# Performance work log

Measured on AMD Instinct MI355X. Metric: run time of the kernel, lower is better.

## Reference

```python
import jax, jax.numpy as jnp
import numpy as np

N_NODES = 100000
N_EDGES = 1600000


def _sage_layer(x, src, dst, Wl, bl, Wr):
    # PyG SAGEConv (aggr='mean', root_weight=True):
    #   out_i = lin_l(mean_{j in N(i)} x_j) + lin_r(x_i)
    msg = x[src]                                              # [E, d] gather
    summed = jax.ops.segment_sum(msg, dst, num_segments=N_NODES)
    cnt = jax.ops.segment_sum(jnp.ones((src.shape[0],), x.dtype), dst,
                              num_segments=N_NODES)
    mean = summed / jnp.maximum(cnt, 1.0)[:, None]            # zero-deg nodes -> 0
    return mean @ Wl + bl + x @ Wr


def setup_inputs() -> dict:
    key = jax.random.key(0)
    ks = jax.random.split(key, 12)
    d_in, d_h, d_out = 6, 128, 64

    def lin(k, fi, fo):
        s = 1.0 / np.sqrt(fi)
        return jax.random.uniform(k, (fi, fo), jnp.float32, -s, s)

    return {
        "x": jax.random.normal(ks[0], (N_NODES, 10), jnp.float32),
        "edge_index": jax.random.randint(ks[1], (2, N_EDGES), 0, N_NODES),
        "Wl0": lin(ks[2], d_in, d_h), "bl0": jnp.zeros((d_h,), jnp.float32),
        "Wr0": lin(ks[3], d_in, d_h),
        "Wl1": lin(ks[4], d_h, d_h), "bl1": jnp.zeros((d_h,), jnp.float32),
        "Wr1": lin(ks[5], d_h, d_h),
        "Wl2": lin(ks[6], d_h, d_out), "bl2": jnp.zeros((d_out,), jnp.float32),
        "Wr2": lin(ks[7], d_h, d_out),
    }


def reference(x, edge_index, Wl0, bl0, Wr0, Wl1, bl1, Wr1, Wl2, bl2, Wr2):
    src, dst = edge_index[0], edge_index[1]
    h = x[:, 4:10]                                            # bus feature slice
    h = jax.nn.relu(_sage_layer(h, src, dst, Wl0, bl0, Wr0))
    h = jax.nn.relu(_sage_layer(h, src, dst, Wl1, bl1, Wr1))
    h = jax.nn.relu(_sage_layer(h, src, dst, Wl2, bl2, Wr2))
    return h
```

## Files before the change

kernel.cpp:

```cpp
#include <hip/hip_runtime.h>


typedef __attribute__((ext_vector_type(8))) short bf16x8;
typedef __attribute__((ext_vector_type(4))) float f32x4;
typedef __attribute__((ext_vector_type(2))) float f32x2;

constexpr int PB = 256;
constexpr int WTCH = 6144;
constexpr float F8SCALE = 32.0f;

static __device__ __forceinline__ int imax(int a, int b) { return a > b ? a : b; }

static __device__ __forceinline__ float bfbits_lo(unsigned u) {
    union { unsigned i; float f; } v; v.i = u << 16; return v.f;
}
static __device__ __forceinline__ float bfbits_hi(unsigned u) {
    union { unsigned i; float f; } v; v.i = u & 0xffff0000u; return v.f;
}
static __device__ __forceinline__ unsigned short f2bf(float f) {
    unsigned u = __float_as_uint(f);
    u = (u + 0x7fffu + ((u >> 16) & 1u)) >> 16;
    return (unsigned short)u;
}
static __device__ __forceinline__ unsigned pack2bf(float a, float b) {
    return (unsigned)f2bf(a) | ((unsigned)f2bf(b) << 16);
}
static __device__ __forceinline__ void acc_f8x4(unsigned u, float* a) {
    f32x2 lo = __builtin_amdgcn_cvt_pk_f32_fp8((int)u, false);
    f32x2 hi = __builtin_amdgcn_cvt_pk_f32_fp8((int)u, true);
    a[0] += lo[0]; a[1] += lo[1]; a[2] += hi[0]; a[3] += hi[1];
}
static __device__ __forceinline__ void acc_bf8(uint4 v, float* a) {
    a[0] += bfbits_lo(v.x); a[1] += bfbits_hi(v.x);
    a[2] += bfbits_lo(v.y); a[3] += bfbits_hi(v.y);
    a[4] += bfbits_lo(v.z); a[5] += bfbits_hi(v.z);
    a[6] += bfbits_lo(v.w); a[7] += bfbits_hi(v.w);
}


static __device__ __forceinline__ void wtfrag_katk(const float* __restrict__ W1,
                                                   const float* __restrict__ W2,
                                                   unsigned short* __restrict__ Wt,
                                                   int K1, int K, int N, int c) {
    int NB = N >> 4;
    int lane = c & 63;
    int n = (c >> 6) % NB;
    int ks = c / (NB << 6);
    int row = n * 16 + (lane & 15);
    int col = ks * 32 + (lane >> 4) * 8;
    unsigned short o[8];
#pragma unroll
    for (int j = 0; j < 8; ++j) {
        int k = col + j;
        float v = (k < K1) ? W1[k * N + row] : W2[(k - K1) * N + row];
        o[j] = f2bf(v);
    }
    *(uint4*)(Wt + (size_t)c * 8) = *(const uint4*)o;
}

static __device__ __forceinline__ void wtfrag_natn(const float* __restrict__ Wa,
                                                   const float* __restrict__ Wb,
                                                   unsigned short* __restrict__ Wt,
                                                   int K, int Nh, int c) {
    int NB = (2 * Nh) >> 4;
    int lane = c & 63;
    int n = (c >> 6) % NB;
    int ks = c / (NB << 6);
    int row = n * 16 + (lane & 15);
    int col = ks * 32 + (lane >> 4) * 8;
    unsigned short o[8];
#pragma unroll
    for (int j = 0; j < 8; ++j) {
        int k = col + j;
        float v = (row < Nh) ? Wa[k * Nh + row] : Wb[k * Nh + (row - Nh)];
        o[j] = f2bf(v);
    }
    *(uint4*)(Wt + (size_t)c * 8) = *(const uint4*)o;
}


__global__ __launch_bounds__(256) void k_prep(const float* __restrict__ Wl1,
                                              const float* __restrict__ Wr1,
                                              const float* __restrict__ Wl2,
                                              const float* __restrict__ Wr2,
                                              unsigned short* __restrict__ Wt1,
                                              unsigned short* __restrict__ Wt2,
                                              const int* __restrict__ dst,
                                              int* __restrict__ C,
                                              int nE, int nbk, int epb) {
    if (blockIdx.x < 24) {
        int c = blockIdx.x * 256 + threadIdx.x;
        if (c < 4096)        wtfrag_katk(Wl1, Wr1, Wt1, 128, 256, 128, c);
        else if (c < WTCH)   wtfrag_natn(Wl2, Wr2, Wt2, 128, 64, c - 4096);
        return;
    }
    __shared__ int h[512];
    int b = blockIdx.x - 24;
    for (int i = threadIdx.x; i < nbk; i += 256) h[i] = 0;
    __syncthreads();
    int e0 = b * epb;
    int e1 = min(e0 + epb, nE);
    for (int i = e0 + threadIdx.x; i < e1; i += 256)
        atomicAdd(&h[dst[i] >> 8], 1);
    __syncthreads();
    for (int i = threadIdx.x; i < nbk; i += 256)
        C[b * nbk + i] = h[i];
}


__global__ __launch_bounds__(256) void k_colscan(int* __restrict__ C,
                                                 int* __restrict__ tot, int nbk) {
    __shared__ int sm[256];
    int k = blockIdx.x, t = threadIdx.x;
    int v = C[t * nbk + k];
    sm[t] = v;
    __syncthreads();
    for (int o = 1; o < 256; o <<= 1) {
        int u = (t >= o) ? sm[t - o] : 0;
        __syncthreads();
        sm[t] += u;
        __syncthreads();
    }
    C[t * nbk + k] = sm[t] - v;
    if (t == 255) tot[k] = sm[255];
}

__global__ __launch_bounds__(256) void k_scan_a(const int* __restrict__ cnt,
                                                int* __restrict__ offs, int n) {
    __shared__ int sm[256];
    int t = threadIdx.x;
    int base = t * 4;
    int v0 = 0, v1 = 0, v2 = 0, v3 = 0;
    if (base + 3 < n) {
        int4 q = *(const int4*)(cnt + base);
        v0 = q.x; v1 = q.y; v2 = q.z; v3 = q.w;
    } else {
        if (base < n)     v0 = cnt[base];
        if (base + 1 < n) v1 = cnt[base + 1];
        if (base + 2 < n) v2 = cnt[base + 2];
    }
    int s = v0 + v1 + v2 + v3;
    sm[t] = s;
    __syncthreads();
    for (int o = 1; o < 256; o <<= 1) {
        int u = (t >= o) ? sm[t - o] : 0;
        __syncthreads();
        sm[t] += u;
        __syncthreads();
    }
    int excl = sm[t] - s;
    if (base < n)     offs[base]     = excl;
    if (base + 1 < n) offs[base + 1] = excl + v0;
    if (base + 2 < n) offs[base + 2] = excl + v0 + v1;
    if (base + 3 < n) offs[base + 3] = excl + v0 + v1 + v2;
    if (t == 255) offs[n] = sm[255];
}

__global__ __launch_bounds__(256) void k_p1fill(const int* __restrict__ src,
                                                const int* __restrict__ dst,
                                                const int* __restrict__ bstart,
                                                const int* __restrict__ C,
                                                unsigned* __restrict__ ebuf,
                                                int nE, int nbk, int epb) {
    __shared__ int cur[512];
    int b = blockIdx.x;
    for (int i = threadIdx.x; i < nbk; i += 256)
        cur[i] = bstart[i] + C[b * nbk + i];
    __syncthreads();
    int e0 = b * epb;
    int e1 = min(e0 + epb, nE);
    for (int i = e0 + threadIdx.x; i < e1; i += 256) {
        int d = dst[i];
        unsigned s = (unsigned)src[i];
        int p = atomicAdd(&cur[d >> 8], 1);
        ebuf[p] = (s << 8) | (unsigned)(d & 255);
    }
}

__global__ __launch_bounds__(256) void k_p2fill(const unsigned* __restrict__ ebuf,
                                                const int* __restrict__ bstart,
                                                int* __restrict__ offs,
                                                int* __restrict__ csr,
                                                int nN, int nE) {
    __shared__ int h[256], sm[256], cur[256];
    int k = blockIdx.x, t = threadIdx.x;
    int base = bstart[k], end = bstart[k + 1];
    h[t] = 0;
    __syncthreads();
    for (int i = base + t; i < end; i += 256)
        atomicAdd(&h[ebuf[i] & 255u], 1);
    __syncthreads();
    int v = h[t];
    sm[t] = v;
    __syncthreads();
    for (int o = 1; o < 256; o <<= 1) {
        int u = (t >= o) ? sm[t - o] : 0;
        __syncthreads();
        sm[t] += u;
        __syncthreads();
    }
    int excl = sm[t] - v;
    int node = (k << 8) + t;
    if (node < nN) offs[node] = base + excl;
    cur[t] = base + excl;
    if (k == 0 && t == 0) offs[nN] = nE;
    __syncthreads();
    for (int i = base + t; i < end; i += 256) {
        unsigned e = ebuf[i];
        int p = atomicAdd(&cur[e & 255u], 1);
        csr[p] = (int)(e >> 8);
    }
}


__global__ __launch_bounds__(256) void k_l0f(const float* __restrict__ x,
                                             const int* __restrict__ offs,
                                             const int* __restrict__ csr,
                                             const float* __restrict__ Wl,
                                             const float* __restrict__ bl,
                                             const float* __restrict__ Wr,
                                             unsigned short* __restrict__ out,
                                             unsigned char* __restrict__ out8, int nN) {
    int idx = blockIdx.x * 256 + threadIdx.x;
    int node = idx >> 4;
    int j = threadIdx.x & 15;
    if (node >= nN) return;
    int lo = offs[node], hi = offs[node + 1];
    float a0 = 0, a1 = 0, a2 = 0, a3 = 0, a4 = 0, a5 = 0;
    for (int e = lo + j; e < hi; e += 16) {
        int s = csr[e];
        const float* r = x + (size_t)s * 10 + 4;
        float2 v0 = *(const float2*)(r);
        float2 v1 = *(const float2*)(r + 2);
        float2 v2 = *(const float2*)(r + 4);
        a0 += v0.x; a1 += v0.y; a2 += v1.x; a3 += v1.y; a4 += v2.x; a5 += v2.y;
    }
#pragma unroll
    for (int mask = 1; mask < 16; mask <<= 1) {
        a0 += __shfl_xor(a0, mask); a1 += __shfl_xor(a1, mask);
        a2 += __shfl_xor(a2, mask); a3 += __shfl_xor(a3, mask);
        a4 += __shfl_xor(a4, mask); a5 += __shfl_xor(a5, mask);
    }
    float inv = 1.0f / (float)imax(hi - lo, 1);
    float m[6] = {a0 * inv, a1 * inv, a2 * inv, a3 * inv, a4 * inv, a5 * inv};
    const float* hp = x + (size_t)node * 10 + 4;
    float2 h01 = *(const float2*)hp, h23 = *(const float2*)(hp + 2), h45 = *(const float2*)(hp + 4);
    float h[6] = {h01.x, h01.y, h23.x, h23.y, h45.x, h45.y};
    int j0 = j * 8;
    float4 b0 = *(const float4*)(bl + j0);
    float4 b1 = *(const float4*)(bl + j0 + 4);
    float v[8] = {b0.x, b0.y, b0.z, b0.w, b1.x, b1.y, b1.z, b1.w};
#pragma unroll
    for (int k = 0; k < 6; ++k) {
        float4 w0 = *(const float4*)(Wl + k * 128 + j0);
        float4 w1 = *(const float4*)(Wl + k * 128 + j0 + 4);
        v[0] = fmaf(m[k], w0.x, v[0]); v[1] = fmaf(m[k], w0.y, v[1]);
        v[2] = fmaf(m[k], w0.z, v[2]); v[3] = fmaf(m[k], w0.w, v[3]);
        v[4] = fmaf(m[k], w1.x, v[4]); v[5] = fmaf(m[k], w1.y, v[5]);
        v[6] = fmaf(m[k], w1.z, v[6]); v[7] = fmaf(m[k], w1.w, v[7]);
    }
#pragma unroll
    for (int k = 0; k < 6; ++k) {
        float4 w0 = *(const float4*)(Wr + k * 128 + j0);
        float4 w1 = *(const float4*)(Wr + k * 128 + j0 + 4);
        v[0] = fmaf(h[k], w0.x, v[0]); v[1] = fmaf(h[k], w0.y, v[1]);
        v[2] = fmaf(h[k], w0.z, v[2]); v[3] = fmaf(h[k], w0.w, v[3]);
        v[4] = fmaf(h[k], w1.x, v[4]); v[5] = fmaf(h[k], w1.y, v[5]);
        v[6] = fmaf(h[k], w1.z, v[6]); v[7] = fmaf(h[k], w1.w, v[7]);
    }
#pragma unroll
    for (int t = 0; t < 8; ++t) v[t] = fmaxf(v[t], 0.f);
    unsigned ob[4];
#pragma unroll
    for (int t = 0; t < 4; ++t) ob[t] = pack2bf(v[2 * t], v[2 * t + 1]);
    *(uint4*)(out + (size_t)node * 128 + j0) = *(const uint4*)ob;
    int d0 = __builtin_amdgcn_cvt_pk_fp8_f32(v[0] * F8SCALE, v[1] * F8SCALE, 0, false);
    d0     = __builtin_amdgcn_cvt_pk_fp8_f32(v[2] * F8SCALE, v[3] * F8SCALE, d0, true);
    int d1 = __builtin_amdgcn_cvt_pk_fp8_f32(v[4] * F8SCALE, v[5] * F8SCALE, 0, false);
    d1     = __builtin_amdgcn_cvt_pk_fp8_f32(v[6] * F8SCALE, v[7] * F8SCALE, d1, true);
    uint2 o8; o8.x = (unsigned)d0; o8.y = (unsigned)d1;
    *(uint2*)(out8 + (size_t)node * 128 + j0) = o8;
}


__global__ __launch_bounds__(256) void k_agg128f8(const unsigned char* __restrict__ X,
                                                  const int* __restrict__ offs,
                                                  const int* __restrict__ csr,
                                                  unsigned short* __restrict__ M, int nN) {
    int idx = blockIdx.x * 256 + threadIdx.x;
    int node = idx >> 3;
    int fl = idx & 7;
    if (node >= nN) return;
    int lo = offs[node], hi = offs[node + 1];
    float a[16];
#pragma unroll
    for (int j = 0; j < 16; ++j) a[j] = 0.f;
    int e = lo;
    for (; e + 8 <= hi; e += 8) {
        uint4 v0 = *(const uint4*)(X + (size_t)csr[e + 0] * 128 + fl * 16);
        uint4 v1 = *(const uint4*)(X + (size_t)csr[e + 1] * 128 + fl * 16);
        uint4 v2 = *(const uint4*)(X + (size_t)csr[e + 2] * 128 + fl * 16);
        uint4 v3 = *(const uint4*)(X + (size_t)csr[e + 3] * 128 + fl * 16);
        uint4 v4 = *(const uint4*)(X + (size_t)csr[e + 4] * 128 + fl * 16);
        uint4 v5 = *(const uint4*)(X + (size_t)csr[e + 5] * 128 + fl * 16);
        uint4 v6 = *(const uint4*)(X + (size_t)csr[e + 6] * 128 + fl * 16);
        uint4 v7 = *(const uint4*)(X + (size_t)csr[e + 7] * 128 + fl * 16);
        acc_f8x4(v0.x, a + 0); acc_f8x4(v0.y, a + 4); acc_f8x4(v0.z, a + 8); acc_f8x4(v0.w, a + 12);
        acc_f8x4(v1.x, a + 0); acc_f8x4(v1.y, a + 4); acc_f8x4(v1.z, a + 8); acc_f8x4(v1.w, a + 12);
        acc_f8x4(v2.x, a + 0); acc_f8x4(v2.y, a + 4); acc_f8x4(v2.z, a + 8); acc_f8x4(v2.w, a + 12);
        acc_f8x4(v3.x, a + 0); acc_f8x4(v3.y, a + 4); acc_f8x4(v3.z, a + 8); acc_f8x4(v3.w, a + 12);
        acc_f8x4(v4.x, a + 0); acc_f8x4(v4.y, a + 4); acc_f8x4(v4.z, a + 8); acc_f8x4(v4.w, a + 12);
        acc_f8x4(v5.x, a + 0); acc_f8x4(v5.y, a + 4); acc_f8x4(v5.z, a + 8); acc_f8x4(v5.w, a + 12);
        acc_f8x4(v6.x, a + 0); acc_f8x4(v6.y, a + 4); acc_f8x4(v6.z, a + 8); acc_f8x4(v6.w, a + 12);
        acc_f8x4(v7.x, a + 0); acc_f8x4(v7.y, a + 4); acc_f8x4(v7.z, a + 8); acc_f8x4(v7.w, a + 12);
    }
    for (; e + 4 <= hi; e += 4) {
        uint4 v0 = *(const uint4*)(X + (size_t)csr[e + 0] * 128 + fl * 16);
        uint4 v1 = *(const uint4*)(X + (size_t)csr[e + 1] * 128 + fl * 16);
        uint4 v2 = *(const uint4*)(X + (size_t)csr[e + 2] * 128 + fl * 16);
        uint4 v3 = *(const uint4*)(X + (size_t)csr[e + 3] * 128 + fl * 16);
        acc_f8x4(v0.x, a + 0); acc_f8x4(v0.y, a + 4); acc_f8x4(v0.z, a + 8); acc_f8x4(v0.w, a + 12);
        acc_f8x4(v1.x, a + 0); acc_f8x4(v1.y, a + 4); acc_f8x4(v1.z, a + 8); acc_f8x4(v1.w, a + 12);
        acc_f8x4(v2.x, a + 0); acc_f8x4(v2.y, a + 4); acc_f8x4(v2.z, a + 8); acc_f8x4(v2.w, a + 12);
        acc_f8x4(v3.x, a + 0); acc_f8x4(v3.y, a + 4); acc_f8x4(v3.z, a + 8); acc_f8x4(v3.w, a + 12);
    }
    for (; e < hi; ++e) {
        uint4 v = *(const uint4*)(X + (size_t)csr[e] * 128 + fl * 16);
        acc_f8x4(v.x, a + 0); acc_f8x4(v.y, a + 4); acc_f8x4(v.z, a + 8); acc_f8x4(v.w, a + 12);
    }
    float inv = 1.0f / (F8SCALE * (float)imax(hi - lo, 1));
    unsigned o[8];
#pragma unroll
    for (int j = 0; j < 8; ++j) o[j] = pack2bf(a[2 * j] * inv, a[2 * j + 1] * inv);
    unsigned short* mp = M + (size_t)node * 128 + fl * 16;
    *(uint4*)(mp)     = *(const uint4*)(o);
    *(uint4*)(mp + 8) = *(const uint4*)(o + 4);
}

__global__ __launch_bounds__(256) void k_agg64f(const unsigned short* __restrict__ X,
                                                const int* __restrict__ offs,
                                                const int* __restrict__ csr,
                                                const float* __restrict__ y2,
                                                const float* __restrict__ bl2,
                                                float* __restrict__ out, int nN) {
    int idx = blockIdx.x * 256 + threadIdx.x;
    int node = idx >> 3;
    int fl = idx & 7;
    if (node >= nN) return;
    int lo = offs[node], hi = offs[node + 1];
    float a[8] = {0, 0, 0, 0, 0, 0, 0, 0};
    int e = lo;
    for (; e + 8 <= hi; e += 8) {
        uint4 v0 = *(const uint4*)(X + (size_t)csr[e + 0] * 64 + fl * 8);
        uint4 v1 = *(const uint4*)(X + (size_t)csr[e + 1] * 64 + fl * 8);
        uint4 v2 = *(const uint4*)(X + (size_t)csr[e + 2] * 64 + fl * 8);
        uint4 v3 = *(const uint4*)(X + (size_t)csr[e + 3] * 64 + fl * 8);
        uint4 v4 = *(const uint4*)(X + (size_t)csr[e + 4] * 64 + fl * 8);
        uint4 v5 = *(const uint4*)(X + (size_t)csr[e + 5] * 64 + fl * 8);
        uint4 v6 = *(const uint4*)(X + (size_t)csr[e + 6] * 64 + fl * 8);
        uint4 v7 = *(const uint4*)(X + (size_t)csr[e + 7] * 64 + fl * 8);
        acc_bf8(v0, a); acc_bf8(v1, a); acc_bf8(v2, a); acc_bf8(v3, a);
        acc_bf8(v4, a); acc_bf8(v5, a); acc_bf8(v6, a); acc_bf8(v7, a);
    }
    for (; e + 4 <= hi; e += 4) {
        uint4 v0 = *(const uint4*)(X + (size_t)csr[e + 0] * 64 + fl * 8);
        uint4 v1 = *(const uint4*)(X + (size_t)csr[e + 1] * 64 + fl * 8);
        uint4 v2 = *(const uint4*)(X + (size_t)csr[e + 2] * 64 + fl * 8);
        uint4 v3 = *(const uint4*)(X + (size_t)csr[e + 3] * 64 + fl * 8);
        acc_bf8(v0, a); acc_bf8(v1, a); acc_bf8(v2, a); acc_bf8(v3, a);
    }
    for (; e < hi; ++e) {
        uint4 v = *(const uint4*)(X + (size_t)csr[e] * 64 + fl * 8);
        acc_bf8(v, a);
    }
    float inv = 1.0f / (float)imax(hi - lo, 1);
    const float* yp = y2 + (size_t)node * 64 + fl * 8;
    float4 ya = *(const float4*)yp;
    float4 yb = *(const float4*)(yp + 4);
    float4 ba = *(const float4*)(bl2 + fl * 8);
    float4 bb = *(const float4*)(bl2 + fl * 8 + 4);
    float* o = out + (size_t)node * 64 + fl * 8;
    *(float4*)(o) = make_float4(fmaxf(fmaf(a[0], inv, ya.x + ba.x), 0.f),
                                fmaxf(fmaf(a[1], inv, ya.y + ba.y), 0.f),
                                fmaxf(fmaf(a[2], inv, ya.z + ba.z), 0.f),
                                fmaxf(fmaf(a[3], inv, ya.w + ba.w), 0.f));
    *(float4*)(o + 4) = make_float4(fmaxf(fmaf(a[4], inv, yb.x + bb.x), 0.f),
                                    fmaxf(fmaf(a[5], inv, yb.y + bb.y), 0.f),
                                    fmaxf(fmaf(a[6], inv, yb.z + bb.z), 0.f),
                                    fmaxf(fmaf(a[7], inv, yb.w + bb.w), 0.f));
}


template <int KA, int KB, int N>
__global__ __launch_bounds__(256) void k_mfma(const unsigned short* __restrict__ A0,
                                              const unsigned short* __restrict__ A1,
                                              const unsigned short* __restrict__ Wt,
                                              const float* __restrict__ bias,
                                              unsigned short* __restrict__ Cout, int nN) {
    constexpr int K = KA + KB;
    constexpr int NSTEP = K / 32;
    constexpr int NB = N / 16;
    const int tid = threadIdx.x;
    const int wave = (blockIdx.x * 256 + tid) >> 6;
    const int m0 = wave * 32;
    if (m0 >= nN) return;
    const int lane = tid & 63;
    const int lr = lane & 15;
    const int lk = lane >> 4;

    f32x4 acc[2][NB];
#pragma unroll
    for (int g = 0; g < 2; ++g)
#pragma unroll
        for (int n = 0; n < NB; ++n) acc[g][n] = (f32x4){0.f, 0.f, 0.f, 0.f};

    auto loadA = [&](int kk, bf16x8& a0, bf16x8& a1) {
        const unsigned short* Ap;
        int lda, krel;
        if (KB > 0 && kk >= KA) { Ap = A1; lda = KB; krel = kk - KA; }
        else                    { Ap = A0; lda = KA; krel = kk; }
        a0 = *(const bf16x8*)(Ap + (size_t)(m0 + lr) * lda + krel + lk * 8);
        a1 = *(const bf16x8*)(Ap + (size_t)(m0 + 16 + lr) * lda + krel + lk * 8);
    };
    auto loadB = [&](int ks, bf16x8* b) {
        const unsigned short* Wk = Wt + (((size_t)ks * NB) << 6) * 8 + lane * 8;
#pragma unroll
        for (int n = 0; n < NB; ++n)
            b[n] = *(const bf16x8*)(Wk + ((size_t)n << 6) * 8);
    };

    bf16x8 a0c, a1c, a0n, a1n;
    bf16x8 bc[NB], bn[NB];
    loadA(0, a0c, a1c);
    loadB(0, bc);

#pragma unroll
    for (int ks = 0; ks < NSTEP; ++ks) {
        if (ks + 1 < NSTEP) {
            loadA((ks + 1) * 32, a0n, a1n);
            loadB(ks + 1, bn);
        }
#pragma unroll
        for (int n = 0; n < NB; ++n) {
            acc[0][n] = __builtin_amdgcn_mfma_f32_16x16x32_bf16(a0c, bc[n], acc[0][n], 0, 0, 0);
            acc[1][n] = __builtin_amdgcn_mfma_f32_16x16x32_bf16(a1c, bc[n], acc[1][n], 0, 0, 0);
        }
        if (ks + 1 < NSTEP) {
            a0c = a0n; a1c = a1n;
#pragma unroll
            for (int n = 0; n < NB; ++n) bc[n] = bn[n];
        }
    }

#pragma unroll
    for (int g = 0; g < 2; ++g) {
#pragma unroll
        for (int r = 0; r < 4; ++r) {
            int gm = m0 + g * 16 + lk * 4 + r;
#pragma unroll
            for (int n = 0; n < NB; ++n) {
                float v = fmaxf(acc[g][n][r] + bias[n * 16 + lr], 0.f);
                Cout[(size_t)gm * N + n * 16 + lr] = f2bf(v);
            }
        }
    }
}


__global__ __launch_bounds__(256) void k_mfma_l2(const unsigned short* __restrict__ A0,
                                                 const unsigned short* __restrict__ Wt,
                                                 unsigned short* __restrict__ z2,
                                                 float* __restrict__ y2, int nN) {
    constexpr int K = 128, NSTEP = 4, NB = 8;
    const int tid = threadIdx.x;
    const int wave = (blockIdx.x * 256 + tid) >> 6;
    const int m0 = wave * 32;
    if (m0 >= nN) return;
    const int lane = tid & 63;
    const int lr = lane & 15;
    const int lk = lane >> 4;

    f32x4 acc[2][NB];
#pragma unroll
    for (int g = 0; g < 2; ++g)
#pragma unroll
        for (int n = 0; n < NB; ++n) acc[g][n] = (f32x4){0.f, 0.f, 0.f, 0.f};

    auto loadA = [&](int kk, bf16x8& a0, bf16x8& a1) {
        a0 = *(const bf16x8*)(A0 + (size_t)(m0 + lr) * K + kk + lk * 8);
        a1 = *(const bf16x8*)(A0 + (size_t)(m0 + 16 + lr) * K + kk + lk * 8);
    };
    auto loadB = [&](int ks, bf16x8* b) {
        const unsigned short* Wk = Wt + (((size_t)ks * NB) << 6) * 8 + lane * 8;
#pragma unroll
        for (int n = 0; n < NB; ++n)
            b[n] = *(const bf16x8*)(Wk + ((size_t)n << 6) * 8);
    };

    bf16x8 a0c, a1c, a0n, a1n;
    bf16x8 bc[NB], bn[NB];
    loadA(0, a0c, a1c);
    loadB(0, bc);

#pragma unroll
    for (int ks = 0; ks < NSTEP; ++ks) {
        if (ks + 1 < NSTEP) {
            loadA((ks + 1) * 32, a0n, a1n);
            loadB(ks + 1, bn);
        }
#pragma unroll
        for (int n = 0; n < NB; ++n) {
            acc[0][n] = __builtin_amdgcn_mfma_f32_16x16x32_bf16(a0c, bc[n], acc[0][n], 0, 0, 0);
            acc[1][n] = __builtin_amdgcn_mfma_f32_16x16x32_bf16(a1c, bc[n], acc[1][n], 0, 0, 0);
        }
        if (ks + 1 < NSTEP) {
            a0c = a0n; a1c = a1n;
#pragma unroll
            for (int n = 0; n < NB; ++n) bc[n] = bn[n];
        }
    }

#pragma unroll
    for (int g = 0; g < 2; ++g) {
#pragma unroll
        for (int r = 0; r < 4; ++r) {
            int gm = m0 + g * 16 + lk * 4 + r;
#pragma unroll
            for (int n = 0; n < 4; ++n)
                z2[(size_t)gm * 64 + n * 16 + lr] = f2bf(acc[g][n][r]);
#pragma unroll
            for (int n = 4; n < 8; ++n)
                y2[(size_t)gm * 64 + (n - 4) * 16 + lr] = acc[g][n][r];
        }
    }
}


extern "C" void kernel_launch(void* const* d_in, const int* in_sizes, int n_in,
                              void* d_out, int out_size, void* d_ws, size_t ws_size,
                              hipStream_t stream) {
    const float* x   = (const float*)d_in[0];
    const int*   ei  = (const int*)d_in[1];
    const float* Wl0 = (const float*)d_in[2];
    const float* bl0 = (const float*)d_in[3];
    const float* Wr0 = (const float*)d_in[4];
    const float* Wl1 = (const float*)d_in[5];
    const float* bl1 = (const float*)d_in[6];
    const float* Wr1 = (const float*)d_in[7];
    const float* Wl2 = (const float*)d_in[8];
    const float* bl2 = (const float*)d_in[9];
    const float* Wr2 = (const float*)d_in[10];

    const int nN = in_sizes[0] / 10;
    const int nE = in_sizes[1] / 2;
    const int* src = ei;
    const int* dst = ei + nE;
    const int nbk = (nN + 255) >> 8;
    const int epb = (nE + PB - 1) / PB;

    char* ws = (char*)d_ws;
    size_t off = 0;
    auto alloc = [&](size_t bytes) -> char* {
        char* p = ws + off;
        off = (off + bytes + 255) & ~(size_t)255;
        return p;
    };
    unsigned short* out0   = (unsigned short*)alloc((size_t)nN * 128 * 2);
    unsigned char*  out0f8 = (unsigned char*)alloc((size_t)nN * 128);
    unsigned short* mean1  = (unsigned short*)alloc((size_t)nN * 128 * 2);
    unsigned short* out1   = (unsigned short*)alloc((size_t)nN * 128 * 2);
    unsigned short* Wt1 = (unsigned short*)alloc((size_t)128 * 256 * 2);
    unsigned short* Wt2 = (unsigned short*)alloc((size_t)128 * 128 * 2);
    int* C      = (int*)alloc((size_t)PB * nbk * 4);
    int* tot    = (int*)alloc((size_t)nbk * 4);
    int* bstart = (int*)alloc(((size_t)nbk + 1) * 4);
    int* offs   = (int*)alloc(((size_t)nN + 1) * 4);
    int* csr    = (int*)alloc((size_t)nE * 4);
    unsigned* ebuf = (unsigned*)alloc((size_t)nE * 4);

    unsigned short* z2 = out0;
    float*          y2 = (float*)mean1;

    k_prep<<<24 + PB, 256, 0, stream>>>(Wl1, Wr1, Wl2, Wr2, Wt1, Wt2, dst, C, nE, nbk, epb);
    k_colscan<<<nbk, 256, 0, stream>>>(C, tot, nbk);
    k_scan_a<<<1, 256, 0, stream>>>(tot, bstart, nbk);
    k_p1fill<<<PB, 256, 0, stream>>>(src, dst, bstart, C, ebuf, nE, nbk, epb);
    k_p2fill<<<nbk, 256, 0, stream>>>(ebuf, bstart, offs, csr, nN, nE);

    k_l0f<<<((size_t)nN * 16 + 255) / 256, 256, 0, stream>>>(
        x, offs, csr, Wl0, bl0, Wr0, out0, out0f8, nN);

    const int gemm_grid = (nN / 32 + 3) / 4 + 1;

    k_agg128f8<<<((size_t)nN * 8 + 255) / 256, 256, 0, stream>>>(out0f8, offs, csr, mean1, nN);
    k_mfma<128, 128, 128><<<gemm_grid, 256, 0, stream>>>(mean1, out0, Wt1, bl1, out1, nN);

    k_mfma_l2<<<gemm_grid, 256, 0, stream>>>(out1, Wt2, z2, y2, nN);
    k_agg64f<<<((size_t)nN * 8 + 255) / 256, 256, 0, stream>>>(
        z2, offs, csr, y2, bl2, (float*)d_out, nN);
}
```

Before: 198.8 us.

## Fuse CSR build kernels into one cooperative kernel with grid syncs

Replaces the five separate CSR-construction launches (histogram/weight prep, column scan, bucket scan, pass-1 fill, pass-2 fill) with a single cooperative kernel that separates phases with grid.sync(). This is meant to remove per-launch overhead and inter-kernel gaps in the graph preprocessing. The cost is grid-wide barriers, a grid size of max(nbk, 280) blocks that must all be co-resident, and blocks sitting idle in phases where only some of them work.

After: 393.5 us. 1.98x slower.

```diff
diff --git a/kernel.cpp b/kernel.cpp
--- a/kernel.cpp
+++ b/kernel.cpp
@@ -1,4 +1,7 @@
 #include <hip/hip_runtime.h>
+#include <hip/hip_cooperative_groups.h>
+
+namespace cg = cooperative_groups;
 
 
 typedef __attribute__((ext_vector_type(8))) short bf16x8;
@@ -79,136 +82,128 @@
 }
 
 
-__global__ __launch_bounds__(256) void k_prep(const float* __restrict__ Wl1,
-                                              const float* __restrict__ Wr1,
-                                              const float* __restrict__ Wl2,
-                                              const float* __restrict__ Wr2,
-                                              unsigned short* __restrict__ Wt1,
-                                              unsigned short* __restrict__ Wt2,
-                                              const int* __restrict__ dst,
-                                              int* __restrict__ C,
-                                              int nE, int nbk, int epb) {
-    if (blockIdx.x < 24) {
-        int c = blockIdx.x * 256 + threadIdx.x;
-        if (c < 4096)        wtfrag_katk(Wl1, Wr1, Wt1, 128, 256, 128, c);
-        else if (c < WTCH)   wtfrag_natn(Wl2, Wr2, Wt2, 128, 64, c - 4096);
-        return;
-    }
-    __shared__ int h[512];
-    int b = blockIdx.x - 24;
-    for (int i = threadIdx.x; i < nbk; i += 256) h[i] = 0;
-    __syncthreads();
-    int e0 = b * epb;
-    int e1 = min(e0 + epb, nE);
-    for (int i = e0 + threadIdx.x; i < e1; i += 256)
-        atomicAdd(&h[dst[i] >> 8], 1);
-    __syncthreads();
-    for (int i = threadIdx.x; i < nbk; i += 256)
-        C[b * nbk + i] = h[i];
-}
-
-
-__global__ __launch_bounds__(256) void k_colscan(int* __restrict__ C,
-                                                 int* __restrict__ tot, int nbk) {
-    __shared__ int sm[256];
-    int k = blockIdx.x, t = threadIdx.x;
-    int v = C[t * nbk + k];
-    sm[t] = v;
-    __syncthreads();
-    for (int o = 1; o < 256; o <<= 1) {
-        int u = (t >= o) ? sm[t - o] : 0;
-        __syncthreads();
-        sm[t] += u;
-        __syncthreads();
-    }
-    C[t * nbk + k] = sm[t] - v;
-    if (t == 255) tot[k] = sm[255];
-}
-
-__global__ __launch_bounds__(256) void k_scan_a(const int* __restrict__ cnt,
-                                                int* __restrict__ offs, int n) {
-    __shared__ int sm[256];
-    int t = threadIdx.x;
-    int base = t * 4;
-    int v0 = 0, v1 = 0, v2 = 0, v3 = 0;
-    if (base + 3 < n) {
-        int4 q = *(const int4*)(cnt + base);
-        v0 = q.x; v1 = q.y; v2 = q.z; v3 = q.w;
-    } else {
-        if (base < n)     v0 = cnt[base];
-        if (base + 1 < n) v1 = cnt[base + 1];
-        if (base + 2 < n) v2 = cnt[base + 2];
-    }
-    int s = v0 + v1 + v2 + v3;
-    sm[t] = s;
-    __syncthreads();
-    for (int o = 1; o < 256; o <<= 1) {
-        int u = (t >= o) ? sm[t - o] : 0;
-        __syncthreads();
-        sm[t] += u;
-        __syncthreads();
-    }
-    int excl = sm[t] - s;
-    if (base < n)     offs[base]     = excl;
-    if (base + 1 < n) offs[base + 1] = excl + v0;
-    if (base + 2 < n) offs[base + 2] = excl + v0 + v1;
-    if (base + 3 < n) offs[base + 3] = excl + v0 + v1 + v2;
-    if (t == 255) offs[n] = sm[255];
-}
-
-__global__ __launch_bounds__(256) void k_p1fill(const int* __restrict__ src,
-                                                const int* __restrict__ dst,
-                                                const int* __restrict__ bstart,
-                                                const int* __restrict__ C,
-                                                unsigned* __restrict__ ebuf,
-                                                int nE, int nbk, int epb) {
-    __shared__ int cur[512];
-    int b = blockIdx.x;
-    for (int i = threadIdx.x; i < nbk; i += 256)
-        cur[i] = bstart[i] + C[b * nbk + i];
-    __syncthreads();
-    int e0 = b * epb;
-    int e1 = min(e0 + epb, nE);
-    for (int i = e0 + threadIdx.x; i < e1; i += 256) {
-        int d = dst[i];
-        unsigned s = (unsigned)src[i];
-        int p = atomicAdd(&cur[d >> 8], 1);
-        ebuf[p] = (s << 8) | (unsigned)(d & 255);
-    }
-}
-
-__global__ __launch_bounds__(256) void k_p2fill(const unsigned* __restrict__ ebuf,
-                                                const int* __restrict__ bstart,
-                                                int* __restrict__ offs,
-                                                int* __restrict__ csr,
-                                                int nN, int nE) {
-    __shared__ int h[256], sm[256], cur[256];
-    int k = blockIdx.x, t = threadIdx.x;
-    int base = bstart[k], end = bstart[k + 1];
-    h[t] = 0;
-    __syncthreads();
-    for (int i = base + t; i < end; i += 256)
-        atomicAdd(&h[ebuf[i] & 255u], 1);
-    __syncthreads();
-    int v = h[t];
-    sm[t] = v;
-    __syncthreads();
-    for (int o = 1; o < 256; o <<= 1) {
-        int u = (t >= o) ? sm[t - o] : 0;
-        __syncthreads();
-        sm[t] += u;
-        __syncthreads();
-    }
-    int excl = sm[t] - v;
-    int node = (k << 8) + t;
-    if (node < nN) offs[node] = base + excl;
-    cur[t] = base + excl;
-    if (k == 0 && t == 0) offs[nN] = nE;
-    __syncthreads();
-    for (int i = base + t; i < end; i += 256) {
-        unsigned e = ebuf[i];
-        int p = atomicAdd(&cur[e & 255u], 1);
-        csr[p] = (int)(e >> 8);
+__global__ __launch_bounds__(256) void k_build(const float* __restrict__ Wl1,
+                                               const float* __restrict__ Wr1,
+                                               const float* __restrict__ Wl2,
+                                               const float* __restrict__ Wr2,
+                                               unsigned short* __restrict__ Wt1,
+                                               unsigned short* __restrict__ Wt2,
+                                               const int* __restrict__ src,
+                                               const int* __restrict__ dst,
+                                               int* __restrict__ C,
+                                               int* __restrict__ tot,
+                                               int* __restrict__ bstart,
+                                               int* __restrict__ offs,
+                                               int* __restrict__ csr,
+                                               unsigned* __restrict__ ebuf,
+                                               int nN, int nE, int nbk, int epb) {
+    cg::grid_group grid = cg::this_grid();
+    __shared__ int sh[768];
+    const int b = blockIdx.x, t = threadIdx.x;
+
+    if (b < 24) {
+        int c = b * 256 + t;
+        if (c < 4096)      wtfrag_katk(Wl1, Wr1, Wt1, 128, 256, 128, c);
+        else if (c < WTCH) wtfrag_natn(Wl2, Wr2, Wt2, 128, 64, c - 4096);
+    } else if (b < 24 + PB) {
+        int bb = b - 24;
+        for (int i = t; i < nbk; i += 256) sh[i] = 0;
+        __syncthreads();
+        int e0 = bb * epb, e1 = min(e0 + epb, nE);
+        for (int i = e0 + t; i < e1; i += 256)
+            atomicAdd(&sh[dst[i] >> 8], 1);
+        __syncthreads();
+        for (int i = t; i < nbk; i += 256)
+            C[bb * nbk + i] = sh[i];
+    }
+    grid.sync();
+
+    if (b < nbk) {
+        int v = C[t * nbk + b];
+        sh[t] = v;
+        __syncthreads();
+        for (int o = 1; o < 256; o <<= 1) {
+            int u = (t >= o) ? sh[t - o] : 0;
+            __syncthreads();
+            sh[t] += u;
+            __syncthreads();
+        }
+        C[t * nbk + b] = sh[t] - v;
+        if (t == 255) tot[b] = sh[255];
+    }
+    grid.sync();
+
+    if (b == 0) {
+        int base = t * 4;
+        int v0 = 0, v1 = 0, v2 = 0, v3 = 0;
+        if (base + 3 < nbk) {
+            int4 q = *(const int4*)(tot + base);
+            v0 = q.x; v1 = q.y; v2 = q.z; v3 = q.w;
+        } else {
+            if (base < nbk)     v0 = tot[base];
+            if (base + 1 < nbk) v1 = tot[base + 1];
+            if (base + 2 < nbk) v2 = tot[base + 2];
+        }
+        int s = v0 + v1 + v2 + v3;
+        sh[t] = s;
+        __syncthreads();
+        for (int o = 1; o < 256; o <<= 1) {
+            int u = (t >= o) ? sh[t - o] : 0;
+            __syncthreads();
+            sh[t] += u;
+            __syncthreads();
+        }
+        int excl = sh[t] - s;
+        if (base < nbk)     bstart[base]     = excl;
+        if (base + 1 < nbk) bstart[base + 1] = excl + v0;
+        if (base + 2 < nbk) bstart[base + 2] = excl + v0 + v1;
+        if (base + 3 < nbk) bstart[base + 3] = excl + v0 + v1 + v2;
+        if (t == 255) bstart[nbk] = sh[255];
+    }
+    grid.sync();
+
+    if (b < PB) {
+        for (int i = t; i < nbk; i += 256)
+            sh[i] = bstart[i] + C[b * nbk + i];
+        __syncthreads();
+        int e0 = b * epb, e1 = min(e0 + epb, nE);
+        for (int i = e0 + t; i < e1; i += 256) {
+            int d = dst[i];
+            unsigned s = (unsigned)src[i];
+            int p = atomicAdd(&sh[d >> 8], 1);
+            ebuf[p] = (s << 8) | (unsigned)(d & 255);
+        }
+    }
+    grid.sync();
+
+    if (b < nbk) {
+        int base = bstart[b], end = bstart[b + 1];
+        int* h = sh; int* sm = sh + 256; int* cur = sh + 512;
+        h[t] = 0;
+        __syncthreads();
+        for (int i = base + t; i < end; i += 256)
+            atomicAdd(&h[ebuf[i] & 255u], 1);
+        __syncthreads();
+        int v = h[t];
+        sm[t] = v;
+        __syncthreads();
+        for (int o = 1; o < 256; o <<= 1) {
+            int u = (t >= o) ? sm[t - o] : 0;
+            __syncthreads();
+            sm[t] += u;
+            __syncthreads();
+        }
+        int excl = sm[t] - v;
+        int node = (b << 8) + t;
+        if (node < nN) offs[node] = base + excl;
+        cur[t] = base + excl;
+        if (b == 0 && t == 0) offs[nN] = nE;
+        __syncthreads();
+        for (int i = base + t; i < end; i += 256) {
+            unsigned e = ebuf[i];
+            int p = atomicAdd(&cur[e & 255u], 1);
+            csr[p] = (int)(e >> 8);
+        }
     }
 }
 
@@ -551,12 +546,12 @@
     const float* bl2 = (const float*)d_in[9];
     const float* Wr2 = (const float*)d_in[10];
 
-    const int nN = in_sizes[0] / 10;
-    const int nE = in_sizes[1] / 2;
+    int nN = in_sizes[0] / 10;
+    int nE = in_sizes[1] / 2;
     const int* src = ei;
     const int* dst = ei + nE;
-    const int nbk = (nN + 255) >> 8;
-    const int epb = (nE + PB - 1) / PB;
+    int nbk = (nN + 255) >> 8;
+    int epb = (nE + PB - 1) / PB;
 
     char* ws = (char*)d_ws;
     size_t off = 0;
@@ -581,11 +576,14 @@
     unsigned short* z2 = out0;
     float*          y2 = (float*)mean1;
 
-    k_prep<<<24 + PB, 256, 0, stream>>>(Wl1, Wr1, Wl2, Wr2, Wt1, Wt2, dst, C, nE, nbk, epb);
-    k_colscan<<<nbk, 256, 0, stream>>>(C, tot, nbk);
-    k_scan_a<<<1, 256, 0, stream>>>(tot, bstart, nbk);
-    k_p1fill<<<PB, 256, 0, stream>>>(src, dst, bstart, C, ebuf, nE, nbk, epb);
-    k_p2fill<<<nbk, 256, 0, stream>>>(ebuf, bstart, offs, csr, nN, nE);
+    int gb = (nbk > 24 + PB) ? nbk : (24 + PB);
+    void* bargs[] = {(void*)&Wl1, (void*)&Wr1, (void*)&Wl2, (void*)&Wr2,
+                     (void*)&Wt1, (void*)&Wt2, (void*)&src, (void*)&dst,
+                     (void*)&C, (void*)&tot, (void*)&bstart, (void*)&offs,
+                     (void*)&csr, (void*)&ebuf,
+                     (void*)&nN, (void*)&nE, (void*)&nbk, (void*)&epb};
+    hipLaunchCooperativeKernel((const void*)k_build, dim3(gb), dim3(256),
+                               bargs, 0, stream);
 
     k_l0f<<<((size_t)nN * 16 + 255) / 256, 256, 0, stream>>>(
         x, offs, csr, Wl0, bl0, Wr0, out0, out0f8, nN);
```
